# Kernel tuning notes

Measured on AMD Instinct MI355X. Metric: run time of the kernel, lower is better.

The kernel has to match this reference:

```python
import jax, jax.numpy as jnp
import numpy as np

B, P, K, H = 8, 4096, 20, 128  # graphs, points per graph, kNN, hidden_channels


def _linear_init(key, fin, fout):
    s = 1.0 / np.sqrt(fin)
    kw, kb = jax.random.split(key)
    W = jax.random.uniform(kw, (fin, fout), jnp.float32, -s, s)
    b = jax.random.uniform(kb, (fout,), jnp.float32, -s, s)
    return W, b


def setup_inputs() -> dict:
    key = jax.random.key(0)
    ks = jax.random.split(key, 6)
    x = jax.random.normal(ks[0], (B, P, 3), jnp.float32)
    W1, b1 = _linear_init(ks[1], 2 * 3, H)
    W2, b2 = _linear_init(ks[2], 2 * H, H)
    W3, b3 = _linear_init(ks[3], 2 * H, H)
    W4, b4 = _linear_init(ks[4], H, H)
    W5, b5 = _linear_init(ks[5], H, 3)
    return dict(x=x, W1=W1, b1=b1, W2=W2, b2=b2, W3=W3, b3=b3,
                W4=W4, b4=b4, W5=W5, b5=b5)


def _dynamic_edge_conv(x, W, b):
    # x: [B, P, D]. Recompute kNN graph in feature space, EdgeConv with max aggr.
    sq = jnp.sum(x * x, axis=-1)                                   # [B, P]
    d2 = sq[:, :, None] + sq[:, None, :] - 2.0 * jnp.einsum('bid,bjd->bij', x, x)
    eye = jnp.eye(x.shape[1], dtype=bool)                          # exclude self-loops
    d2 = jnp.where(eye[None], jnp.inf, d2)
    _, idx = jax.lax.top_k(-d2, K)                                 # [B, P, K]
    xj = jax.vmap(lambda xb, ib: xb[ib])(x, idx)                   # [B, P, K, D] gather
    xi = jnp.broadcast_to(x[:, :, None, :], xj.shape)
    e = jnp.concatenate([xi, xj - xi], axis=-1)                    # [B, P, K, 2D]
    h = jax.nn.relu(e @ W + b)                                     # edge MLP
    return jnp.max(h, axis=2)                                      # max aggregation -> [B, P, H]


def reference(x, W1, b1, W2, b2, W3, b3, W4, b4, W5, b5):
    h = jax.nn.relu(_dynamic_edge_conv(x, W1, b1))
    h = jax.nn.relu(_dynamic_edge_conv(h, W2, b2))
    h = jax.nn.relu(_dynamic_edge_conv(h, W3, b3))
    g = jnp.mean(h, axis=1)                                        # global_mean_pool -> [B, H]
    g = jax.nn.relu(g @ W4 + b4)
    # dropout is identity in eval mode
    return g @ W5 + b5                                             # [B, 3]
```

## Files before the change

kernel.cpp:

```cpp
#include <hip/hip_runtime.h>
#include <hip/hip_bf16.h>


static constexpr int B_ = 8, P_ = 4096, K_ = 20, H_ = 128;
static constexpr float FINF = 3.0e38f;
static constexpr int CAPH = 192;

typedef __attribute__((ext_vector_type(8))) short short8;
typedef __attribute__((ext_vector_type(16))) float floatx16;

__device__ __forceinline__ float dist3(float x0, float x1, float x2,
                                       const float4& v) {
  return fmaf(-2.f, fmaf(x0, v.x, fmaf(x1, v.y, x2 * v.z)), v.w);
}

__device__ __forceinline__ void cvt_split(float v, ushort& h, ushort& l) {
  __hip_bfloat16 hb = __float2bfloat16(v);
  float hf = __bfloat162float(hb);
  __hip_bfloat16 lb = __float2bfloat16(v - hf);
  h = *(ushort*)&hb;
  l = *(ushort*)&lb;
}

__device__ __forceinline__ float kth20_par4(float* v, int lane) {
  const int sub = lane & 3;
  for (int r = 0; r < 12; ++r) {
    float lm = v[0];
    int la = 0;
#pragma unroll
    for (int t = 1; t < 8; ++t) {
      if (v[t] > lm) { lm = v[t]; la = t; }
    }
    int gid = sub * 8 + la;
#pragma unroll
    for (int off = 1; off < 4; off <<= 1) {
      float om = __shfl_xor(lm, off);
      int oid = __shfl_xor(gid, off);
      if (om > lm || (om == lm && oid > gid)) { lm = om; gid = oid; }
    }
    if ((gid >> 3) == sub) v[gid & 7] = -FINF;
  }
  float lm = v[0];
#pragma unroll
  for (int t = 1; t < 8; ++t) lm = fmaxf(lm, v[t]);
#pragma unroll
  for (int off = 1; off < 4; off <<= 1) lm = fmaxf(lm, __shfl_xor(lm, off));
  return lm;
}

__global__ __launch_bounds__(256) void feat3p_kernel(
    const float* __restrict__ X, const float* __restrict__ W,
    const float* __restrict__ bias, float* __restrict__ c_out,
    float* __restrict__ u_out, float4* __restrict__ pt4) {
  const int h = threadIdx.x & (H_ - 1);
  const int pg = threadIdx.x >> 7;
  const int bb = blockIdx.x & 7;
  const int pb = blockIdx.x >> 3;
  const int pbase = bb * P_ + pb * 8;
  const int p0 = pbase + pg * 4;
  if (threadIdx.x < 8) {
    const float* row = X + (size_t)(pbase + threadIdx.x) * 3;
    float4 v;
    v.x = row[0]; v.y = row[1]; v.z = row[2];
    v.w = fmaf(v.x, v.x, fmaf(v.y, v.y, v.z * v.z));
    pt4[pbase + threadIdx.x] = v;
  }
  float a0 = 0, a1 = 0, a2 = 0, a3 = 0, u0 = 0, u1 = 0, u2 = 0, u3 = 0;
  const float* xp = X + (size_t)p0 * 3;
#pragma unroll
  for (int d = 0; d < 3; ++d) {
    float wt = W[d * H_ + h];
    float wb = W[(3 + d) * H_ + h];
    float x0 = xp[d], x1 = xp[3 + d], x2 = xp[6 + d], x3 = xp[9 + d];
    a0 = fmaf(x0, wt, a0); u0 = fmaf(x0, wb, u0);
    a1 = fmaf(x1, wt, a1); u1 = fmaf(x1, wb, u1);
    a2 = fmaf(x2, wt, a2); u2 = fmaf(x2, wb, u2);
    a3 = fmaf(x3, wt, a3); u3 = fmaf(x3, wb, u3);
  }
  float bv = bias[h];
  c_out[(size_t)(p0 + 0) * H_ + h] = a0 - u0 + bv;
  c_out[(size_t)(p0 + 1) * H_ + h] = a1 - u1 + bv;
  c_out[(size_t)(p0 + 2) * H_ + h] = a2 - u2 + bv;
  c_out[(size_t)(p0 + 3) * H_ + h] = a3 - u3 + bv;
  u_out[(size_t)(p0 + 0) * H_ + h] = u0;
  u_out[(size_t)(p0 + 1) * H_ + h] = u1;
  u_out[(size_t)(p0 + 2) * H_ + h] = u2;
  u_out[(size_t)(p0 + 3) * H_ + h] = u3;
}

__global__ __launch_bounds__(256) void wprep2_kernel(
    const float* __restrict__ W2, const float* __restrict__ W3,
    ushort* __restrict__ Vfh2, ushort* __restrict__ Vfl2,
    ushort* __restrict__ Vfh3, ushort* __restrict__ Vfl3) {
  const int which = blockIdx.x >> 4;
  const float* W = which ? W3 : W2;
  ushort* Vfh = which ? Vfh3 : Vfh2;
  ushort* Vfl = which ? Vfl3 : Vfl2;
  int tid = (blockIdx.x & 15) * 256 + threadIdx.x;
  int t = tid >> 9;
  int s = (tid >> 6) & 7;
  int lane = tid & 63;
  int col = t * 32 + (lane & 31);
  int kb = s * 16 + ((lane >> 5) << 3);
  ushort h[8], l[8];
#pragma unroll
  for (int e = 0; e < 8; ++e) {
    int k = kb + e;
    float v;
    if (col < 128) v = W[k * H_ + col] - W[(128 + k) * H_ + col];
    else v = W[(128 + k) * H_ + col - 128];
    cvt_split(v, h[e], l[e]);
  }
  size_t off = (size_t)((t * 8 + s) * 64 + lane) * 8;
  *(short8*)(Vfh + off) = *(short8*)h;
  *(short8*)(Vfl + off) = *(short8*)l;
}

__device__ __forceinline__ void stage_async(const ushort* __restrict__ Xhi,
                                            const ushort* __restrict__ Xlo,
                                            size_t tile, char* buf, int w,
                                            int lane) {
  const char* gh = (const char*)(Xhi + tile);
  const char* gl = (const char*)(Xlo + tile);
  const int lo16 = lane * 16;
#pragma unroll
  for (int it = 0; it < 4; ++it) {
    const int off = (w * 4 + it) * 1024;
    __builtin_amdgcn_global_load_lds(
        (const __attribute__((address_space(1))) void*)(gh + off + lo16),
        (__attribute__((address_space(3))) void*)(buf + off), 16, 0, 0);
    __builtin_amdgcn_global_load_lds(
        (const __attribute__((address_space(1))) void*)(gl + off + lo16),
        (__attribute__((address_space(3))) void*)(buf + 16384 + off), 16, 0, 0);
  }
}

__device__ __forceinline__ void stage_async32(const ushort* __restrict__ Xhi,
                                              const ushort* __restrict__ Xlo,
                                              size_t tile, char* buf, int w,
                                              int lane) {
  const char* gh = (const char*)(Xhi + tile);
  const char* gl = (const char*)(Xlo + tile);
  const int lo16 = lane * 16;
#pragma unroll
  for (int it = 0; it < 4; ++it) {
    const int off = (w * 4 + it) * 1024;
    __builtin_amdgcn_global_load_lds(
        (const __attribute__((address_space(1))) void*)(gh + off + lo16),
        (__attribute__((address_space(3))) void*)(buf + off), 16, 0, 0);
    __builtin_amdgcn_global_load_lds(
        (const __attribute__((address_space(1))) void*)(gl + off + lo16),
        (__attribute__((address_space(3))) void*)(buf + 8192 + off), 16, 0, 0);
  }
}

__device__ __forceinline__ void load_afrag_sw(const ushort* __restrict__ X,
                                              size_t gb, int row, int lane,
                                              short8* a) {
  const ushort* base = X + (gb + row) * (size_t)H_;
  const int x = row & 15;
  const int kh = lane >> 5;
#pragma unroll
  for (int s = 0; s < 8; ++s) {
    a[s] = *(const short8*)(base + (((s * 2 + kh) ^ x) << 3));
  }
}

__device__ __forceinline__ floatx16 gram32(const char* lds, const short8* ahi,
                                           const short8* alo, int jh,
                                           int lane) {
  floatx16 a0, a1, a2;
#pragma unroll
  for (int i = 0; i < 16; ++i) { a0[i] = 0.f; a1[i] = 0.f; a2[i] = 0.f; }
  const int base = (jh * 32 + (lane & 31)) * 256;
  const int kh = lane >> 5;
  const int x = lane & 15;
#pragma unroll
  for (int s = 0; s < 8; ++s) {
    const int off = base + (((s * 2 + kh) ^ x) << 4);
    short8 bh = *(const short8*)(lds + off);
    short8 bl = *(const short8*)(lds + 16384 + off);
    a0 = __builtin_amdgcn_mfma_f32_32x32x16_bf16(ahi[s], bh, a0, 0, 0, 0);
    a1 = __builtin_amdgcn_mfma_f32_32x32x16_bf16(ahi[s], bl, a1, 0, 0, 0);
    a2 = __builtin_amdgcn_mfma_f32_32x32x16_bf16(alo[s], bh, a2, 0, 0, 0);
  }
  floatx16 acc;
#pragma unroll
  for (int i = 0; i < 16; ++i) acc[i] = (a0[i] + a1[i]) + a2[i];
  return acc;
}

__device__ __forceinline__ floatx16 gram32t(const char* lds, const short8* ahi,
                                            const short8* alo, int lane) {
  floatx16 a0, a1, a2;
#pragma unroll
  for (int i = 0; i < 16; ++i) { a0[i] = 0.f; a1[i] = 0.f; a2[i] = 0.f; }
  const int base = (lane & 31) * 256;
  const int kh = lane >> 5;
  const int x = lane & 15;
#pragma unroll
  for (int s = 0; s < 8; ++s) {
    const int off = base + (((s * 2 + kh) ^ x) << 4);
    short8 bh = *(const short8*)(lds + off);
    short8 bl = *(const short8*)(lds + 8192 + off);
    a0 = __builtin_amdgcn_mfma_f32_32x32x16_bf16(ahi[s], bh, a0, 0, 0, 0);
    a1 = __builtin_amdgcn_mfma_f32_32x32x16_bf16(ahi[s], bl, a1, 0, 0, 0);
    a2 = __builtin_amdgcn_mfma_f32_32x32x16_bf16(alo[s], bh, a2, 0, 0, 0);
  }
  floatx16 acc;
#pragma unroll
  for (int i = 0; i < 16; ++i) acc[i] = (a0[i] + a1[i]) + a2[i];
  return acc;
}

__global__ __launch_bounds__(256) void featpart_kernel(
    const ushort* __restrict__ Xhi, const ushort* __restrict__ Xlo,
    const ushort* __restrict__ Vfh, const ushort* __restrict__ Vfl,
    const float* __restrict__ bias, float* __restrict__ c_out,
    float* __restrict__ u_out, const float* __restrict__ sqn,
    float* __restrict__ tau) {
  __shared__ char buf[32768];
  __shared__ float ldist[64 * 65];

  const int tid = threadIdx.x;
  const int lane = tid & 63;
  const int w = tid >> 6;
  const int rh = w >> 1, jh = w & 1;
  const int b = blockIdx.x & 7;
  const int i0 = (blockIdx.x >> 3) * 64;
  const size_t gb = (size_t)b * P_;

  short8 ahi[8], alo[8];
  const int arow = i0 + rh * 32 + (lane & 31);
  load_afrag_sw(Xhi, gb, arow, lane, ahi);
  load_afrag_sw(Xlo, gb, arow, lane, alo);

  const int rl = 4 * (lane >> 5);
#pragma unroll
  for (int tt = 0; tt < 4; ++tt) {
    const int t = jh * 4 + tt;
    floatx16 a0, a1, a2;
#pragma unroll
    for (int i = 0; i < 16; ++i) { a0[i] = 0.f; a1[i] = 0.f; a2[i] = 0.f; }
#pragma unroll
    for (int s = 0; s < 8; ++s) {
      const size_t off = (size_t)((t * 8 + s) * 64 + lane) * 8;
      short8 bh = *(const short8*)(Vfh + off);
      short8 bl = *(const short8*)(Vfl + off);
      a0 = __builtin_amdgcn_mfma_f32_32x32x16_bf16(ahi[s], bh, a0, 0, 0, 0);
      a1 = __builtin_amdgcn_mfma_f32_32x32x16_bf16(ahi[s], bl, a1, 0, 0, 0);
      a2 = __builtin_amdgcn_mfma_f32_32x32x16_bf16(alo[s], bh, a2, 0, 0, 0);
    }
    const int col = t * 32 + (lane & 31);
    if (jh == 0) {
      float bv = bias[col];
#pragma unroll
      for (int g = 0; g < 16; ++g) {
        int row = i0 + rh * 32 + rl + (g & 3) + 8 * (g >> 2);
        c_out[(gb + row) * (size_t)H_ + col] = ((a0[g] + a1[g]) + a2[g]) + bv;
      }
    } else {
#pragma unroll
      for (int g = 0; g < 16; ++g) {
        int row = i0 + rh * 32 + rl + (g & 3) + 8 * (g >> 2);
        u_out[(gb + row) * (size_t)H_ + col - 128] = (a0[g] + a1[g]) + a2[g];
      }
    }
  }

  const int rowb = rh * 32 + rl;
  const int jcol = jh * 32 + (lane & 31);
  const int srow = tid >> 2;
  const int sr = tid & 3;
  const int gi = i0 + srow;
  float bd[8];

#pragma unroll
  for (int ch = 0; ch < 8; ++ch) {
    const int tb = ch * 64;
    stage_async(Xhi, Xlo, (gb + tb) * (size_t)H_, buf, w, lane);
    float sqv = sqn[gb + tb + jcol];
    __syncthreads();
    floatx16 acc = gram32(buf, ahi, alo, jh, lane);
#pragma unroll
    for (int g = 0; g < 16; ++g) {
      ldist[(rowb + (g & 3) + 8 * (g >> 2)) * 65 + jcol] =
          fmaf(-2.f, acc[g], sqv);
    }
    __syncthreads();
    const float* drow = ldist + srow * 65 + sr * 16;
    float m = FINF;
#pragma unroll
    for (int jj = 0; jj < 16; ++jj) {
      float s = drow[jj];
      int jg = tb + sr * 16 + jj;
      m = (jg == gi) ? m : fminf(m, s);
    }
    bd[ch] = m;
  }
  float t20 = kth20_par4(bd, lane);
  if (sr == 0) tau[gb + gi] = t20;
}

__global__ __launch_bounds__(128) void knn_compact_kernel(
    const ushort* __restrict__ Xhi, const ushort* __restrict__ Xlo,
    const float* __restrict__ sqn, const float* __restrict__ tau,
    float2* __restrict__ cand, int* __restrict__ cnt) {
  __shared__ char buf[2][16384];

  const int tid = threadIdx.x;
  const int lane = tid & 63;
  const int w = tid >> 6;
  const int b = blockIdx.x & 7;
  const int rest = blockIdx.x >> 3;
  const int half = rest & 1;
  const int i0 = (rest >> 1) * 64;
  const size_t gb = (size_t)b * P_;

  short8 ahi[8], alo[8];
  const int arow = i0 + w * 32 + (lane & 31);
  load_afrag_sw(Xhi, gb, arow, lane, ahi);
  load_afrag_sw(Xlo, gb, arow, lane, alo);

  const int rowb = i0 + w * 32 + 4 * (lane >> 5);
  float taur[16];
  int cur[16];
#pragma unroll
  for (int g = 0; g < 16; ++g) {
    taur[g] = tau[gb + rowb + (g & 3) + 8 * (g >> 2)];
    cur[g] = 0;
  }
  float2* candrow = cand + (gb + rowb) * (size_t)(2 * CAPH) + half * CAPH;
  const unsigned lmask = (1u << (lane & 31)) - 1u;
  const int jbase = half * 2048;

  stage_async32(Xhi, Xlo, (gb + jbase) * (size_t)H_, buf[0], w, lane);
  float sqv_next = sqn[gb + jbase + (lane & 31)];

  for (int c = 0; c < 64; ++c) {
    const int tb = jbase + c * 32;
    __syncthreads();
    float sqv = sqv_next;
    if (c < 63) {
      stage_async32(Xhi, Xlo, (gb + tb + 32) * (size_t)H_, buf[(c + 1) & 1], w,
                    lane);
      sqv_next = sqn[gb + tb + 32 + (lane & 31)];
    }
    floatx16 acc = gram32t(buf[c & 1], ahi, alo, lane);
    const int jg = tb + (lane & 31);
#pragma unroll
    for (int g = 0; g < 16; ++g) {
      float d = fmaf(-2.f, acc[g], sqv);
      bool pred = (d <= taur[g]);
      unsigned long long mk = __ballot(pred);
      if (mk) {
        unsigned seg = (lane >= 32) ? (unsigned)(mk >> 32) : (unsigned)mk;
        int idx = cur[g] + __popc(seg & lmask);
        if (pred && idx < CAPH) {
          float2 e;
          e.x = d;
          e.y = __int_as_float(jg);
          candrow[(size_t)((g & 3) + 8 * (g >> 2)) * (2 * CAPH) + idx] = e;
        }
        cur[g] += __popc(seg);
      }
    }
  }
  if ((lane & 31) == 0) {
#pragma unroll
    for (int g = 0; g < 16; ++g) {
      int row = rowb + (g & 3) + 8 * (g >> 2);
      cnt[(gb + row) * 2 + half] = cur[g] < CAPH ? cur[g] : CAPH;
    }
  }
}

__global__ __launch_bounds__(256) void knn3_full_kernel(
    const float4* __restrict__ pt4, float2* __restrict__ cand,
    int* __restrict__ cnt) {
  __shared__ float ltau[64];
  const int tid = threadIdx.x;
  const int b = blockIdx.x & 7;
  const int i0 = (blockIdx.x >> 3) * 64;
  const size_t gb = (size_t)b * P_;

  {
    const int row_local = tid >> 2;
    const int r = tid & 3;
    const int gi = i0 + row_local;
    float4 pi = pt4[gb + gi];
    const float4* pg = pt4 + gb + r * 256;
    float bd[8];
#pragma unroll
    for (int s = 0; s < 8; ++s) {
      float m = FINF;
#pragma unroll 4
      for (int jj = 0; jj < 32; ++jj) {
        int jl = s * 32 + jj;
        float4 v = pg[jl];
        float d = dist3(pi.x, pi.y, pi.z, v);
        int jg = r * 256 + jl;
        m = (jg == gi) ? m : fminf(m, d);
      }
      bd[s] = m;
    }
    float t20 = kth20_par4(bd, tid & 63);
    if (r == 0) ltau[row_local] = t20;
  }
  __syncthreads();

  const int lane = tid & 63;
  const int w = tid >> 6;
  const int r0 = i0 + w * 16;
  float xr0[16], xr1[16], xr2[16], taur[16];
  int cur[16];
#pragma unroll
  for (int r = 0; r < 16; ++r) {
    float4 p = pt4[gb + r0 + r];
    xr0[r] = p.x; xr1[r] = p.y; xr2[r] = p.z;
    taur[r] = ltau[w * 16 + r];
    cur[r] = 0;
  }
  const float4* pg = pt4 + gb;
  float4 v = pg[lane];
  for (int ch = 0; ch < 64; ++ch) {
    float4 vn;
    if (ch < 63) vn = pg[(ch + 1) * 64 + lane];
    const int jg = ch * 64 + lane;
#pragma unroll
    for (int r = 0; r < 16; ++r) {
      float d = dist3(xr0[r], xr1[r], xr2[r], v);
      bool pred = (d <= taur[r]);
      unsigned long long mk = __ballot(pred);
      if (mk) {
        int n = __popcll(mk);
        int pre = __popcll(mk & ((1ull << lane) - 1ull));
        int idx = cur[r] + pre;
        if (pred && idx < 2 * CAPH) {
          float2 e;
          e.x = d;
          e.y = __int_as_float(jg);
          cand[(gb + r0 + r) * (size_t)(2 * CAPH) + idx] = e;
        }
        cur[r] += n;
      }
    }
    v = vn;
  }
  if (lane == 0) {
#pragma unroll
    for (int r = 0; r < 16; ++r) {
      cnt[(gb + r0 + r) * 2] = cur[r] < 2 * CAPH ? cur[r] : 2 * CAPH;
      cnt[(gb + r0 + r) * 2 + 1] = 0;
    }
  }
}

__global__ __launch_bounds__(256) void selsplit_kernel(
    const float2* __restrict__ cand, const int* __restrict__ cnt,
    const float* __restrict__ c, const float* __restrict__ u,
    float* __restrict__ out, ushort* __restrict__ hi,
    ushort* __restrict__ lo, float* __restrict__ sqn) {
  __shared__ int ljs[4][24];
  __shared__ float aggv[4][128];
  const int w = threadIdx.x >> 6;
  const int lane = threadIdx.x & 63;
  const int b = blockIdx.x & 7;
  const int rowbase = b * P_ + (blockIdx.x >> 3) * 4;
  const int row = rowbase + w;
  const int c0 = cnt[row * 2], c1 = cnt[row * 2 + 1];
  const int ctot = c0 + c1;
  float d[6];
  int j[6];
#pragma unroll
  for (int s = 0; s < 6; ++s) {
    int m = s * 64 + lane;
    bool valid = m < ctot;
    int addr = (m < c0) ? m : (CAPH + m - c0);
    if (!valid) addr = 0;
    float2 e = cand[(size_t)row * (2 * CAPH) + addr];
    d[s] = valid ? e.x : FINF;
    j[s] = __float_as_int(e.y);
  }
  for (int round = 0; round < K_ + 1; ++round) {
    float bm = d[0];
    int bs = 0;
#pragma unroll
    for (int s = 1; s < 6; ++s) {
      if (d[s] < bm) { bm = d[s]; bs = s; }
    }
    int id = (lane << 3) | bs;
#pragma unroll
    for (int off = 1; off < 64; off <<= 1) {
      float od = __shfl_xor(bm, off);
      int oid = __shfl_xor(id, off);
      if (od < bm || (od == bm && oid < id)) { bm = od; id = oid; }
    }
    int owner = id >> 3, os = id & 7;
    if (lane == owner) {
      int jv = 0;
#pragma unroll
      for (int s = 0; s < 6; ++s) {
        if (s == os) { jv = j[s]; d[s] = FINF; }
      }
      ljs[w][round] = jv;
    }
  }
  const float2* c2p = (const float2*)(c + (size_t)row * H_);
  float2 ci = c2p[lane];
  float mx = 0.f, my = 0.f;
#pragma unroll 4
  for (int k = 1; k <= K_; ++k) {
    int jj = ljs[w][k];
    float2 uv = *(const float2*)(u + ((size_t)(b << 12) + jj) * H_ + lane * 2);
    mx = fmaxf(mx, ci.x + uv.x);
    my = fmaxf(my, ci.y + uv.y);
  }
  if (out != nullptr) {
    float2 o;
    o.x = mx; o.y = my;
    *(float2*)(out + (size_t)row * H_ + lane * 2) = o;
  }
  if (hi != nullptr) {
    aggv[w][lane * 2] = mx;
    aggv[w][lane * 2 + 1] = my;
    __syncthreads();
    const int tid = threadIdx.x;
    if (tid < 64) {
      const int r = tid >> 4, m = tid & 15;
      const int rrow = rowbase + r;
      float vv[8];
      float ss = 0.f;
      ushort hh[8], ll[8];
#pragma unroll
      for (int e = 0; e < 8; ++e) {
        vv[e] = aggv[r][m * 8 + e];
        ss = fmaf(vv[e], vv[e], ss);
        cvt_split(vv[e], hh[e], ll[e]);
      }
      size_t dst = ((size_t)rrow << 7) + ((size_t)(m ^ (rrow & 15)) << 3);
      *(short8*)(hi + dst) = *(short8*)hh;
      *(short8*)(lo + dst) = *(short8*)ll;
#pragma unroll
      for (int off = 1; off < 16; off <<= 1) ss += __shfl_xor(ss, off);
      if (m == 0) sqn[rrow] = ss;
    }
  }
}

__global__ __launch_bounds__(128) void pool_kernel(const float* __restrict__ hf,
                                                   float* __restrict__ psum) {
  constexpr int CHUNK = 64;
  int blk = blockIdx.x;
  int b = blk >> 6;
  int chunk = blk & 63;
  int h = threadIdx.x;
  int base = (b << 12) + chunk * CHUNK;
  float acc = 0.f;
#pragma unroll 4
  for (int p = 0; p < CHUNK; ++p) acc += hf[(size_t)(base + p) * H_ + h];
  psum[blk * H_ + h] = acc;
}

__global__ __launch_bounds__(128) void head_kernel(
    const float* __restrict__ psum, const float* __restrict__ W4,
    const float* __restrict__ b4, const float* __restrict__ W5,
    const float* __restrict__ b5, float* __restrict__ out) {
  int b = blockIdx.x, h = threadIdx.x;
  __shared__ float g[H_];
  __shared__ float t[H_];
  float s = 0.f;
#pragma unroll 4
  for (int ch = 0; ch < 64; ++ch) s += psum[(b * 64 + ch) * H_ + h];
  g[h] = s * (1.0f / P_);
  __syncthreads();
  float acc = b4[h];
#pragma unroll 4
  for (int d = 0; d < H_; ++d) acc = fmaf(g[d], W4[d * H_ + h], acc);
  t[h] = fmaxf(acc, 0.f);
  __syncthreads();
  if (h < 3) {
    float o = b5[h];
#pragma unroll 4
    for (int d = 0; d < H_; ++d) o = fmaf(t[d], W5[d * 3 + h], o);
    out[b * 3 + h] = o;
  }
}

extern "C" void kernel_launch(void* const* d_in, const int* in_sizes, int n_in,
                              void* d_out, int out_size, void* d_ws,
                              size_t ws_size, hipStream_t stream) {
  const float* x  = (const float*)d_in[0];
  const float* W1 = (const float*)d_in[1];
  const float* b1 = (const float*)d_in[2];
  const float* W2 = (const float*)d_in[3];
  const float* b2 = (const float*)d_in[4];
  const float* W3 = (const float*)d_in[5];
  const float* b3 = (const float*)d_in[6];
  const float* W4 = (const float*)d_in[7];
  const float* b4 = (const float*)d_in[8];
  const float* W5 = (const float*)d_in[9];
  const float* b5 = (const float*)d_in[10];
  float* out = (float*)d_out;

  char* ws = (char*)d_ws;
  const size_t NF = (size_t)B_ * P_ * H_;
  const size_t NP_ = (size_t)B_ * P_;
  float*  bufA = (float*)ws;  ws += NF * 4;
  float*  bufB = (float*)ws;  ws += NF * 4;
  float*  bufU = (float*)ws;  ws += NF * 4;
  ushort* xhi  = (ushort*)ws; ws += NF * 2;
  ushort* xlo  = (ushort*)ws; ws += NF * 2;
  float*  sqn  = (float*)ws;  ws += NP_ * 4;
  float*  psum = (float*)ws;  ws += (size_t)B_ * 64 * H_ * 4;
  float*  tau  = (float*)ws;  ws += NP_ * 4;
  int*    cnt  = (int*)ws;    ws += NP_ * 2 * 4;
  float4* pt4  = (float4*)ws; ws += NP_ * 16;
  ushort* vfh2 = (ushort*)ws; ws += 32768 * 2;
  ushort* vfl2 = (ushort*)ws; ws += 32768 * 2;
  ushort* vfh3 = (ushort*)ws; ws += 32768 * 2;
  ushort* vfl3 = (ushort*)ws; ws += 32768 * 2;
  float2* cand = (float2*)ws; ws += NP_ * (size_t)(2 * CAPH) * 8;

  const int NP = B_ * P_;
  dim3 blk256(256), blk128(128);

  wprep2_kernel<<<32, blk256, 0, stream>>>(W2, W3, vfh2, vfl2, vfh3, vfl3);

  feat3p_kernel<<<NP / 8, blk256, 0, stream>>>(x, W1, b1, bufA, bufU, pt4);
  knn3_full_kernel<<<B_ * 64, blk256, 0, stream>>>(pt4, cand, cnt);
  selsplit_kernel<<<NP / 4, blk256, 0, stream>>>(cand, cnt, bufA, bufU,
                                                 nullptr, xhi, xlo, sqn);

  featpart_kernel<<<B_ * 64, blk256, 0, stream>>>(xhi, xlo, vfh2, vfl2, b2,
                                                  bufB, bufU, sqn, tau);
  knn_compact_kernel<<<B_ * 64 * 2, blk128, 0, stream>>>(xhi, xlo, sqn, tau,
                                                         cand, cnt);
  selsplit_kernel<<<NP / 4, blk256, 0, stream>>>(cand, cnt, bufB, bufU,
                                                 nullptr, xhi, xlo, sqn);

  featpart_kernel<<<B_ * 64, blk256, 0, stream>>>(xhi, xlo, vfh3, vfl3, b3,
                                                  bufB, bufU, sqn, tau);
  knn_compact_kernel<<<B_ * 64 * 2, blk128, 0, stream>>>(xhi, xlo, sqn, tau,
                                                         cand, cnt);
  selsplit_kernel<<<NP / 4, blk256, 0, stream>>>(cand, cnt, bufB, bufU,
                                                 bufA, nullptr, nullptr,
                                                 nullptr);

  pool_kernel<<<B_ * 64, blk128, 0, stream>>>(bufA, psum);
  head_kernel<<<B_, blk128, 0, stream>>>(psum, W4, b4, W5, b5, out);
}
```

Before: 919.7 us.

## Fuse threshold estimation and kNN candidate compaction into one kernel per layer

Merges the featpart kernel (features plus per-row kNN threshold estimate) with the knn_compact kernel, so the threshold stays in LDS and the A fragments already held in registers are reused. This removes one launch per layer, the tau round trip through global memory, and the reload of A fragments. In exchange the fused kernel uses 64KB of LDS with 256 threads and has half as many blocks as the old compact launch (512 instead of 1024), which may lower occupancy and parallelism in the long compaction loop.

```diff
diff --git a/kernel.cpp b/kernel.cpp
--- a/kernel.cpp
+++ b/kernel.cpp
@@ -137,14 +137,14 @@
 
 __device__ __forceinline__ void stage_async32(const ushort* __restrict__ Xhi,
                                               const ushort* __restrict__ Xlo,
-                                              size_t tile, char* buf, int w,
+                                              size_t tile, char* buf, int ws,
                                               int lane) {
   const char* gh = (const char*)(Xhi + tile);
   const char* gl = (const char*)(Xlo + tile);
   const int lo16 = lane * 16;
 #pragma unroll
   for (int it = 0; it < 4; ++it) {
-    const int off = (w * 4 + it) * 1024;
+    const int off = (ws * 4 + it) * 1024;
     __builtin_amdgcn_global_load_lds(
         (const __attribute__((address_space(1))) void*)(gh + off + lo16),
         (__attribute__((address_space(3))) void*)(buf + off), 16, 0, 0);
@@ -213,14 +213,16 @@
   return acc;
 }
 
-__global__ __launch_bounds__(256) void featpart_kernel(
+__global__ __launch_bounds__(256) void featcomp_kernel(
     const ushort* __restrict__ Xhi, const ushort* __restrict__ Xlo,
     const ushort* __restrict__ Vfh, const ushort* __restrict__ Vfl,
     const float* __restrict__ bias, float* __restrict__ c_out,
     float* __restrict__ u_out, const float* __restrict__ sqn,
-    float* __restrict__ tau) {
-  __shared__ char buf[32768];
-  __shared__ float ldist[64 * 65];
+    float2* __restrict__ cand, int* __restrict__ cnt) {
+  __shared__ char smem[65536];
+  char* tbuf = smem;
+  float* ldist = (float*)(smem + 32768);
+  float* ltau = (float*)(smem + 49408);
 
   const int tid = threadIdx.x;
   const int lane = tid & 63;
@@ -268,109 +270,96 @@
     }
   }
 
-  const int rowb = rh * 32 + rl;
-  const int jcol = jh * 32 + (lane & 31);
-  const int srow = tid >> 2;
-  const int sr = tid & 3;
-  const int gi = i0 + srow;
-  float bd[8];
-
-#pragma unroll
-  for (int ch = 0; ch < 8; ++ch) {
-    const int tb = ch * 64;
-    stage_async(Xhi, Xlo, (gb + tb) * (size_t)H_, buf, w, lane);
-    float sqv = sqn[gb + tb + jcol];
-    __syncthreads();
-    floatx16 acc = gram32(buf, ahi, alo, jh, lane);
+  {
+    const int rowb = rh * 32 + rl;
+    const int jcol = jh * 32 + (lane & 31);
+    const int srow = tid >> 2;
+    const int sr = tid & 3;
+    const int gi = i0 + srow;
+    float bd[8];
+#pragma unroll
+    for (int ch = 0; ch < 8; ++ch) {
+      const int tb = ch * 64;
+      stage_async(Xhi, Xlo, (gb + tb) * (size_t)H_, tbuf, w, lane);
+      float sqv = sqn[gb + tb + jcol];
+      __syncthreads();
+      floatx16 acc = gram32(tbuf, ahi, alo, jh, lane);
+#pragma unroll
+      for (int g = 0; g < 16; ++g) {
+        ldist[(rowb + (g & 3) + 8 * (g >> 2)) * 65 + jcol] =
+            fmaf(-2.f, acc[g], sqv);
+      }
+      __syncthreads();
+      const float* drow = ldist + srow * 65 + sr * 16;
+      float m = FINF;
+#pragma unroll
+      for (int jj = 0; jj < 16; ++jj) {
+        float s = drow[jj];
+        int jg = tb + sr * 16 + jj;
+        m = (jg == gi) ? m : fminf(m, s);
+      }
+      bd[ch] = m;
+    }
+    float t20 = kth20_par4(bd, lane);
+    if (sr == 0) ltau[srow] = t20;
+  }
+  __syncthreads();
+
+  {
+    char* sbuf = smem + jh * 32768;
+    const int ws = rh;
+    const int jbase = jh * 2048;
+    const int rowbL = rh * 32 + rl;
+    float taur[16];
+    int cur[16];
 #pragma unroll
     for (int g = 0; g < 16; ++g) {
-      ldist[(rowb + (g & 3) + 8 * (g >> 2)) * 65 + jcol] =
-          fmaf(-2.f, acc[g], sqv);
-    }
-    __syncthreads();
-    const float* drow = ldist + srow * 65 + sr * 16;
-    float m = FINF;
-#pragma unroll
-    for (int jj = 0; jj < 16; ++jj) {
-      float s = drow[jj];
-      int jg = tb + sr * 16 + jj;
-      m = (jg == gi) ? m : fminf(m, s);
-    }
-    bd[ch] = m;
-  }
-  float t20 = kth20_par4(bd, lane);
-  if (sr == 0) tau[gb + gi] = t20;
-}
-
-__global__ __launch_bounds__(128) void knn_compact_kernel(
-    const ushort* __restrict__ Xhi, const ushort* __restrict__ Xlo,
-    const float* __restrict__ sqn, const float* __restrict__ tau,
-    float2* __restrict__ cand, int* __restrict__ cnt) {
-  __shared__ char buf[2][16384];
-
-  const int tid = threadIdx.x;
-  const int lane = tid & 63;
-  const int w = tid >> 6;
-  const int b = blockIdx.x & 7;
-  const int rest = blockIdx.x >> 3;
-  const int half = rest & 1;
-  const int i0 = (rest >> 1) * 64;
-  const size_t gb = (size_t)b * P_;
-
-  short8 ahi[8], alo[8];
-  const int arow = i0 + w * 32 + (lane & 31);
-  load_afrag_sw(Xhi, gb, arow, lane, ahi);
-  load_afrag_sw(Xlo, gb, arow, lane, alo);
-
-  const int rowb = i0 + w * 32 + 4 * (lane >> 5);
-  float taur[16];
-  int cur[16];
-#pragma unroll
-  for (int g = 0; g < 16; ++g) {
-    taur[g] = tau[gb + rowb + (g & 3) + 8 * (g >> 2)];
-    cur[g] = 0;
-  }
-  float2* candrow = cand + (gb + rowb) * (size_t)(2 * CAPH) + half * CAPH;
-  const unsigned lmask = (1u << (lane & 31)) - 1u;
-  const int jbase = half * 2048;
-
-  stage_async32(Xhi, Xlo, (gb + jbase) * (size_t)H_, buf[0], w, lane);
-  float sqv_next = sqn[gb + jbase + (lane & 31)];
-
-  for (int c = 0; c < 64; ++c) {
-    const int tb = jbase + c * 32;
-    __syncthreads();
-    float sqv = sqv_next;
-    if (c < 63) {
-      stage_async32(Xhi, Xlo, (gb + tb + 32) * (size_t)H_, buf[(c + 1) & 1], w,
-                    lane);
-      sqv_next = sqn[gb + tb + 32 + (lane & 31)];
-    }
-    floatx16 acc = gram32t(buf[c & 1], ahi, alo, lane);
-    const int jg = tb + (lane & 31);
-#pragma unroll
-    for (int g = 0; g < 16; ++g) {
-      float d = fmaf(-2.f, acc[g], sqv);
-      bool pred = (d <= taur[g]);
-      unsigned long long mk = __ballot(pred);
-      if (mk) {
-        unsigned seg = (lane >= 32) ? (unsigned)(mk >> 32) : (unsigned)mk;
-        int idx = cur[g] + __popc(seg & lmask);
-        if (pred && idx < CAPH) {
-          float2 e;
-          e.x = d;
-          e.y = __int_as_float(jg);
-          candrow[(size_t)((g & 3) + 8 * (g >> 2)) * (2 * CAPH) + idx] = e;
+      taur[g] = ltau[rowbL + (g & 3) + 8 * (g >> 2)];
+      cur[g] = 0;
+    }
+    float2* candw =
+        cand + (gb + i0 + rh * 32) * (size_t)(2 * CAPH) + jh * CAPH;
+    const int lofs = rl * (2 * CAPH);
+    const unsigned lmask = (1u << (lane & 31)) - 1u;
+
+    stage_async32(Xhi, Xlo, (gb + jbase) * (size_t)H_, sbuf, ws, lane);
+    float sqv_next = sqn[gb + jbase + (lane & 31)];
+
+    for (int c = 0; c < 64; ++c) {
+      const int tb = jbase + c * 32;
+      __syncthreads();
+      float sqv = sqv_next;
+      if (c < 63) {
+        stage_async32(Xhi, Xlo, (gb + tb + 32) * (size_t)H_,
+                      sbuf + (((c + 1) & 1) << 14), ws, lane);
+        sqv_next = sqn[gb + tb + 32 + (lane & 31)];
+      }
+      floatx16 acc = gram32t(sbuf + ((c & 1) << 14), ahi, alo, lane);
+      const int jg = tb + (lane & 31);
+#pragma unroll
+      for (int g = 0; g < 16; ++g) {
+        float d = fmaf(-2.f, acc[g], sqv);
+        bool pred = (d <= taur[g]);
+        unsigned long long mk = __ballot(pred);
+        if (mk) {
+          unsigned seg = (lane >= 32) ? (unsigned)(mk >> 32) : (unsigned)mk;
+          int idx = cur[g] + __popc(seg & lmask);
+          if (pred && idx < CAPH) {
+            float2 e;
+            e.x = d;
+            e.y = __int_as_float(jg);
+            candw[lofs + ((g & 3) + 8 * (g >> 2)) * (2 * CAPH) + idx] = e;
+          }
+          cur[g] += __popc(seg);
         }
-        cur[g] += __popc(seg);
-      }
-    }
-  }
-  if ((lane & 31) == 0) {
-#pragma unroll
-    for (int g = 0; g < 16; ++g) {
-      int row = rowb + (g & 3) + 8 * (g >> 2);
-      cnt[(gb + row) * 2 + half] = cur[g] < CAPH ? cur[g] : CAPH;
+      }
+    }
+    if ((lane & 31) == 0) {
+#pragma unroll
+      for (int g = 0; g < 16; ++g) {
+        int row = i0 + rh * 32 + rl + (g & 3) + 8 * (g >> 2);
+        cnt[(gb + row) * 2 + jh] = cur[g] < CAPH ? cur[g] : CAPH;
+      }
     }
   }
 }
@@ -421,6 +410,7 @@
     taur[r] = ltau[w * 16 + r];
     cur[r] = 0;
   }
+  float2* candw = cand + (gb + r0) * (size_t)(2 * CAPH);
   const float4* pg = pt4 + gb;
   float4 v = pg[lane];
   for (int ch = 0; ch < 64; ++ch) {
@@ -440,7 +430,7 @@
           float2 e;
           e.x = d;
           e.y = __int_as_float(jg);
-          cand[(gb + r0 + r) * (size_t)(2 * CAPH) + idx] = e;
+          candw[r * (2 * CAPH) + idx] = e;
         }
         cur[r] += n;
       }
@@ -613,7 +603,6 @@
   ushort* xlo  = (ushort*)ws; ws += NF * 2;
   float*  sqn  = (float*)ws;  ws += NP_ * 4;
   float*  psum = (float*)ws;  ws += (size_t)B_ * 64 * H_ * 4;
-  float*  tau  = (float*)ws;  ws += NP_ * 4;
   int*    cnt  = (int*)ws;    ws += NP_ * 2 * 4;
   float4* pt4  = (float4*)ws; ws += NP_ * 16;
   ushort* vfh2 = (ushort*)ws; ws += 32768 * 2;
@@ -632,17 +621,13 @@
   selsplit_kernel<<<NP / 4, blk256, 0, stream>>>(cand, cnt, bufA, bufU,
                                                  nullptr, xhi, xlo, sqn);
 
-  featpart_kernel<<<B_ * 64, blk256, 0, stream>>>(xhi, xlo, vfh2, vfl2, b2,
-                                                  bufB, bufU, sqn, tau);
-  knn_compact_kernel<<<B_ * 64 * 2, blk128, 0, stream>>>(xhi, xlo, sqn, tau,
-                                                         cand, cnt);
+  featcomp_kernel<<<B_ * 64, blk256, 0, stream>>>(xhi, xlo, vfh2, vfl2, b2,
+                                                  bufB, bufU, sqn, cand, cnt);
   selsplit_kernel<<<NP / 4, blk256, 0, stream>>>(cand, cnt, bufB, bufU,
                                                  nullptr, xhi, xlo, sqn);
 
-  featpart_kernel<<<B_ * 64, blk256, 0, stream>>>(xhi, xlo, vfh3, vfl3, b3,
-                                                  bufB, bufU, sqn, tau);
-  knn_compact_kernel<<<B_ * 64 * 2, blk128, 0, stream>>>(xhi, xlo, sqn, tau,
-                                                         cand, cnt);
+  featcomp_kernel<<<B_ * 64, blk256, 0, stream>>>(xhi, xlo, vfh3, vfl3, b3,
+                                                  bufB, bufU, sqn, cand, cnt);
   selsplit_kernel<<<NP / 4, blk256, 0, stream>>>(cand, cnt, bufB, bufU,
                                                  bufA, nullptr, nullptr,
                                                  nullptr);
```

Measured after the change: 921.2 us. No clear change (+0.2%).
